# Optimization experiments

Hardware: AMD Instinct MI355X
Metric: run time of the kernel (lower is better)

## Reference

```python
import jax, jax.numpy as jnp
import numpy as np

B, T, E, H = 2, 2048, 1024, 16
Dh = E // H  # head_size = 64


def setup_inputs() -> dict:
    key = jax.random.key(0)
    ks = jax.random.split(key, 6)
    s = E ** -0.5
    x = jax.random.normal(ks[0], (B, T, E), dtype=jnp.float32)
    Wq = jax.random.normal(ks[1], (H, E, Dh), dtype=jnp.float32) * s
    Wk = jax.random.normal(ks[2], (H, E, Dh), dtype=jnp.float32) * s
    Wv = jax.random.normal(ks[3], (H, E, Dh), dtype=jnp.float32) * s
    wo_w = jax.random.normal(ks[4], (E, E), dtype=jnp.float32) * s  # torch Linear weight [out,in]
    wo_b = jax.random.normal(ks[5], (E,), dtype=jnp.float32) * 0.01
    return {"x": x, "Wq": Wq, "Wk": Wk, "Wv": Wv, "wo_w": wo_w, "wo_b": wo_b}


def reference(x, Wq, Wk, Wv, wo_w, wo_b):
    # Batched equivalent of the per-head Python loop: project all heads at once.
    q = jnp.einsum('bte,hed->bhtd', x, Wq)
    k = jnp.einsum('bte,hed->bhtd', x, Wk)
    v = jnp.einsum('bte,hed->bhtd', x, Wv)
    scale = Dh ** -0.5
    scores = jnp.einsum('bhtd,bhsd->bhts', q, k) * scale  # [B,H,T,T]
    causal = jnp.tril(jnp.ones((T, T), dtype=bool))
    scores = jnp.where(causal, scores, jnp.finfo(scores.dtype).min)
    att = jax.nn.softmax(scores, axis=-1)
    out = jnp.einsum('bhts,bhsd->bhtd', att, v)  # [B,H,T,Dh]
    # concat heads (head order along last dim, matching torch.cat over heads)
    out = out.transpose(0, 2, 1, 3).reshape(B, T, E)
    return out @ wo_w.T + wo_b
```

## Files before the change

### kernel.cpp

```cpp
#include <hip/hip_runtime.h>

#define B_ 2
#define T_ 2048
#define E_ 1024
#define H_ 16
#define DH 64

typedef unsigned short u16;
typedef unsigned int u32;
typedef __bf16 bf16x8 __attribute__((ext_vector_type(8)));
typedef float f32x4 __attribute__((ext_vector_type(4)));

__device__ __forceinline__ u16 f2bf(float f) {
  u32 u = __builtin_bit_cast(u32, f);
  u = u + 0x7FFFu + ((u >> 16) & 1u);
  return (u16)(u >> 16);
}
__device__ __forceinline__ bf16x8 ldfrag(const u16* p) { return *(const bf16x8*)p; }

__device__ __forceinline__ void gload_lds16(const u16* g, u16* l) {
  __builtin_amdgcn_global_load_lds((const __attribute__((address_space(1))) u32*)g,
                                   (__attribute__((address_space(3))) u32*)l, 16, 0, 0);
}

__global__ __launch_bounds__(256) void k_conv_all(const float* __restrict__ x,
                                                  const float* __restrict__ Wq,
                                                  const float* __restrict__ Wk,
                                                  const float* __restrict__ Wv,
                                                  const float* __restrict__ wo_w,
                                                  u16* __restrict__ xb, u16* __restrict__ wT,
                                                  u16* __restrict__ woB) {
  __shared__ __align__(16) u16 Ls[64][68];
  const int t = threadIdx.x;
  const int bx = blockIdx.x;
  if (bx < 2048 || bx >= 2816) {
    const float* src = (bx < 2048) ? x : wo_w;
    u16* dst = (bx < 2048) ? xb : woB;
    u32 i = (((bx < 2048) ? bx : (bx - 2816)) * 256u + t) * 8u;
    float4 a = *(const float4*)(src + i);
    float4 b = *(const float4*)(src + i + 4);
    uint4 v;
    v.x = (u32)f2bf(a.x) | ((u32)f2bf(a.y) << 16);
    v.y = (u32)f2bf(a.z) | ((u32)f2bf(a.w) << 16);
    v.z = (u32)f2bf(b.x) | ((u32)f2bf(b.y) << 16);
    v.w = (u32)f2bf(b.z) | ((u32)f2bf(b.w) << 16);
    *(uint4*)(dst + i) = v;
    return;
  }
  const int idx = bx - 2048;
  const int e0 = (idx & 15) * 64;
  const int h = (idx >> 4) & 15;
  const int which = idx >> 8;
  const float* src = (which == 0) ? Wq : ((which == 1) ? Wk : Wv);
  const float scale = (which == 0) ? 0.18033688011112042f : 1.0f;
#pragma unroll
  for (int p = 0; p < 4; p++) {
    int id2 = p * 256 + t;
    int row = id2 >> 4, ch = id2 & 15;
    float4 v = *(const float4*)(src + ((size_t)h * E_ + e0 + row) * DH + ch * 4);
    uint2 pk;
    pk.x = (u32)f2bf(v.x * scale) | ((u32)f2bf(v.y * scale) << 16);
    pk.y = (u32)f2bf(v.z * scale) | ((u32)f2bf(v.w * scale) << 16);
    *(uint2*)(&Ls[row][ch * 4]) = pk;
  }
  __syncthreads();
  u16* dst = wT + ((size_t)which * H_ + h) * (DH * E_);
#pragma unroll
  for (int p = 0; p < 4; p++) {
    int id2 = p * 256 + t;
    int d = id2 >> 4, ec = id2 & 15;
    uint2 pk;
    pk.x = (u32)Ls[ec * 4 + 0][d] | ((u32)Ls[ec * 4 + 1][d] << 16);
    pk.y = (u32)Ls[ec * 4 + 2][d] | ((u32)Ls[ec * 4 + 3][d] << 16);
    *(uint2*)(dst + (size_t)d * E_ + e0 + ec * 4) = pk;
  }
}

__global__ __launch_bounds__(256, 3) void k_qkv(const u16* __restrict__ xb, const u16* __restrict__ wT,
                                                u16* __restrict__ Qb, u16* __restrict__ Kb,
                                                u16* __restrict__ VbT) {
  __shared__ __align__(16) u16 As[128 * 64];
  __shared__ __align__(16) u16 Bs[128 * 64];
  const int tid = threadIdx.x;
  const int w = tid >> 6, lane = tid & 63, quad = lane >> 4, lr = lane & 15;
  const int wr = w >> 1, wc = w & 1;
  const int bid = blockIdx.x;
  const int xcd = bid & 7, bidx = bid >> 3;
  const int t0 = (xcd * 4 + bidx / 24) * 128;
  const int n0 = (bidx % 24) * 128;
  const int sr = lane >> 3, sc = lane & 7;

  f32x4 acc[4][4];
  const f32x4 z4 = {0.f, 0.f, 0.f, 0.f};
#pragma unroll
  for (int i = 0; i < 4; i++)
#pragma unroll
    for (int j = 0; j < 4; j++) acc[i][j] = z4;

  for (int k0 = 0; k0 < E_; k0 += 64) {
    __syncthreads();
#pragma unroll
    for (int ii = 0; ii < 4; ii++) {
      int ra = w * 32 + ii * 8 + sr;
      gload_lds16(xb + (size_t)(t0 + ra) * E_ + k0 + ((sc ^ (ra & 7)) << 3),
                  As + (w * 32 + ii * 8) * 64);
      gload_lds16(wT + (size_t)(n0 + ra) * E_ + k0 + ((sc ^ (ra & 7)) << 3),
                  Bs + (w * 32 + ii * 8) * 64);
    }
    __syncthreads();
#pragma unroll
    for (int kk = 0; kk < 2; kk++) {
      bf16x8 af[4], bfv[4];
#pragma unroll
      for (int rt = 0; rt < 4; rt++) {
        int row = wr * 64 + rt * 16 + lr;
        af[rt] = ldfrag(As + row * 64 + (((kk * 4 + quad) ^ (row & 7)) << 3));
      }
#pragma unroll
      for (int ct = 0; ct < 4; ct++) {
        int row = wc * 64 + ct * 16 + lr;
        bfv[ct] = ldfrag(Bs + row * 64 + (((kk * 4 + quad) ^ (row & 7)) << 3));
      }
#pragma unroll
      for (int rt = 0; rt < 4; rt++)
#pragma unroll
        for (int ct = 0; ct < 4; ct++)
          acc[rt][ct] = __builtin_amdgcn_mfma_f32_16x16x32_bf16(af[rt], bfv[ct], acc[rt][ct], 0, 0, 0);
    }
  }

  const int qkv = n0 >> 10;
  if (qkv < 2) {
    u16* outp = (qkv == 0) ? Qb : Kb;
#pragma unroll
    for (int rt = 0; rt < 4; rt++)
#pragma unroll
      for (int ct = 0; ct < 4; ct++) {
        int n = n0 + wc * 64 + ct * 16 + lr;
        int h = (n >> 6) & 15, d = n & 63;
#pragma unroll
        for (int r = 0; r < 4; r++) {
          int t = t0 + wr * 64 + rt * 16 + quad * 4 + r;
          int bb = t >> 11, tt = t & 2047;
          outp[(((size_t)bb * H_ + h) * T_ + tt) * DH + d] = f2bf(acc[rt][ct][r]);
        }
      }
  } else {
#pragma unroll
    for (int rt = 0; rt < 4; rt++)
#pragma unroll
      for (int ct = 0; ct < 4; ct++) {
        int n = n0 + wc * 64 + ct * 16 + lr;
        int h = (n >> 6) & 15, d = n & 63;
        int t = t0 + wr * 64 + rt * 16 + quad * 4;
        int bb = t >> 11, tt = t & 2047;
        uint2 pk;
        pk.x = (u32)f2bf(acc[rt][ct][0]) | ((u32)f2bf(acc[rt][ct][1]) << 16);
        pk.y = (u32)f2bf(acc[rt][ct][2]) | ((u32)f2bf(acc[rt][ct][3]) << 16);
        *(uint2*)(VbT + (((size_t)bb * H_ + h) * DH + d) * T_ + tt) = pk;
      }
  }
}

__global__ __launch_bounds__(256, 4) void k_attn(const u16* __restrict__ Qb, const u16* __restrict__ Kb,
                                                 const u16* __restrict__ VbT, u16* __restrict__ AO) {
  __shared__ __align__(16) u16 Ks[4096];
  __shared__ __align__(16) u16 Vts[4096];
  __shared__ __align__(16) u16 Ps[4096];
  const int tid = threadIdx.x;
  const int w = tid >> 6, lane = tid & 63, quad = lane >> 4, lr = lane & 15;
  const int l7 = lr & 7;
  const int srow = lane >> 3, schunk = lane & 7;
  const int i = blockIdx.x;
  const int h = blockIdx.y, bb = blockIdx.z;
  const u16* qb = Qb + ((size_t)bb * H_ + h) * (size_t)(T_ * DH);
  const u16* kb = Kb + ((size_t)bb * H_ + h) * (size_t)(T_ * DH);
  const u16* vbT = VbT + ((size_t)bb * H_ + h) * (size_t)(T_ * DH);
  const f32x4 z4 = {0.f, 0.f, 0.f, 0.f};
  const float MFIX = 20.0f;

  for (int jb = 0; jb < 2; jb++) {
    const int qt = jb ? i : (31 - i);
    const int t0 = qt * 64;

    const u16* qrow = qb + (size_t)(t0 + w * 16 + lr) * DH;
    bf16x8 bq0 = ldfrag(qrow + quad * 8);
    bf16x8 bq1 = ldfrag(qrow + 32 + quad * 8);

    f32x4 o_acc[4];
#pragma unroll
    for (int dt = 0; dt < 4; dt++) o_acc[dt] = z4;
    float l_i = 0.f;

    for (int jt = 0; jt <= qt; jt++) {
      const int j0 = jt * 64;
      __syncthreads();
#pragma unroll
      for (int ii = 0; ii < 2; ii++) {
        int r = w * 16 + ii * 8 + srow;
        gload_lds16(kb + (size_t)(j0 + r) * DH + ((schunk ^ (r & 7)) << 3),
                    Ks + (w * 16 + ii * 8) * 64);
        gload_lds16(vbT + (size_t)r * T_ + j0 + ((schunk ^ (r & 7)) << 3),
                    Vts + (w * 16 + ii * 8) * 64);
      }
      __syncthreads();

      f32x4 s_acc[4];
#pragma unroll
      for (int st = 0; st < 4; st++) s_acc[st] = z4;
#pragma unroll
      for (int st = 0; st < 4; st++) {
        bf16x8 ak0 = ldfrag(Ks + (st * 16 + lr) * 64 + ((quad ^ l7) << 3));
        bf16x8 ak1 = ldfrag(Ks + (st * 16 + lr) * 64 + (((4 + quad) ^ l7) << 3));
        s_acc[st] = __builtin_amdgcn_mfma_f32_16x16x32_bf16(ak0, bq0, s_acc[st], 0, 0, 0);
        s_acc[st] = __builtin_amdgcn_mfma_f32_16x16x32_bf16(ak1, bq1, s_acc[st], 0, 0, 0);
      }

      if (jt == qt) {
        int qloc = w * 16 + lr;
#pragma unroll
        for (int st = 0; st < 4; st++) {
          int sbase = st * 16 + quad * 4;
#pragma unroll
          for (int r = 0; r < 4; r++)
            if (sbase + r > qloc) s_acc[st][r] = -__builtin_inff();
        }
      }

      float rsum = 0.f;
#pragma unroll
      for (int st = 0; st < 4; st++) {
        float p0 = __builtin_amdgcn_exp2f(s_acc[st][0] - MFIX);
        float p1 = __builtin_amdgcn_exp2f(s_acc[st][1] - MFIX);
        float p2 = __builtin_amdgcn_exp2f(s_acc[st][2] - MFIX);
        float p3 = __builtin_amdgcn_exp2f(s_acc[st][3] - MFIX);
        rsum += (p0 + p1) + (p2 + p3);
        uint2 pk;
        pk.x = (__builtin_bit_cast(u32, p0) >> 16) | (__builtin_bit_cast(u32, p1) & 0xffff0000u);
        pk.y = (__builtin_bit_cast(u32, p2) >> 16) | (__builtin_bit_cast(u32, p3) & 0xffff0000u);
        *(uint2*)(Ps + (w * 16 + lr) * 64 + (((st * 2 + (quad >> 1)) ^ l7) << 3) + ((quad & 1) << 2)) = pk;
      }
      l_i += rsum;

#pragma unroll
      for (int kk = 0; kk < 2; kk++) {
        bf16x8 bp = ldfrag(Ps + (w * 16 + lr) * 64 + (((kk * 4 + quad) ^ l7) << 3));
#pragma unroll
        for (int dt = 0; dt < 4; dt++) {
          bf16x8 av = ldfrag(Vts + (dt * 16 + lr) * 64 + (((kk * 4 + quad) ^ l7) << 3));
          o_acc[dt] = __builtin_amdgcn_mfma_f32_16x16x32_bf16(av, bp, o_acc[dt], 0, 0, 0);
        }
      }
    }

    l_i += __shfl_xor(l_i, 16);
    l_i += __shfl_xor(l_i, 32);
    float inv = 1.0f / l_i;
    int t = t0 + w * 16 + lr;
    u16* orow = AO + ((size_t)bb * T_ + t) * E_ + h * DH;
#pragma unroll
    for (int dt = 0; dt < 4; dt++) {
      uint2 pk;
      pk.x = (u32)f2bf(o_acc[dt][0] * inv) | ((u32)f2bf(o_acc[dt][1] * inv) << 16);
      pk.y = (u32)f2bf(o_acc[dt][2] * inv) | ((u32)f2bf(o_acc[dt][3] * inv) << 16);
      *(uint2*)(orow + dt * 16 + quad * 4) = pk;
    }
  }
}

__global__ __launch_bounds__(256, 3) void k_oproj(const u16* __restrict__ AO, const u16* __restrict__ woB,
                                                  const float* __restrict__ bias, float* __restrict__ out) {
  __shared__ __align__(16) u16 As[128 * 64];
  __shared__ __align__(16) u16 Bs[64 * 64];
  const int tid = threadIdx.x;
  const int w = tid >> 6, lane = tid & 63, quad = lane >> 4, lr = lane & 15;
  const int wr = w >> 1, wc = w & 1;
  const int bid = blockIdx.x;
  const int xcd = bid & 7, bidx = bid >> 3;
  const int r0 = (xcd * 4 + (bidx >> 4)) * 128;
  const int n0 = (bidx & 15) * 64;
  const int sr = lane >> 3, sc = lane & 7;

  f32x4 acc[4][2];
  const f32x4 z4 = {0.f, 0.f, 0.f, 0.f};
#pragma unroll
  for (int i = 0; i < 4; i++) {
    acc[i][0] = z4;
    acc[i][1] = z4;
  }

  for (int k0 = 0; k0 < E_; k0 += 64) {
    __syncthreads();
#pragma unroll
    for (int ii = 0; ii < 4; ii++) {
      int ra = w * 32 + ii * 8 + sr;
      gload_lds16(AO + (size_t)(r0 + ra) * E_ + k0 + ((sc ^ (ra & 7)) << 3),
                  As + (w * 32 + ii * 8) * 64);
    }
#pragma unroll
    for (int ii = 0; ii < 2; ii++) {
      int rb = w * 16 + ii * 8 + sr;
      gload_lds16(woB + (size_t)(n0 + rb) * E_ + k0 + ((sc ^ (rb & 7)) << 3),
                  Bs + (w * 16 + ii * 8) * 64);
    }
    __syncthreads();
#pragma unroll
    for (int kk = 0; kk < 2; kk++) {
      bf16x8 af[4], bfv[2];
#pragma unroll
      for (int rt = 0; rt < 4; rt++) {
        int row = wr * 64 + rt * 16 + lr;
        af[rt] = ldfrag(As + row * 64 + (((kk * 4 + quad) ^ (row & 7)) << 3));
      }
#pragma unroll
      for (int ct = 0; ct < 2; ct++) {
        int row = wc * 32 + ct * 16 + lr;
        bfv[ct] = ldfrag(Bs + row * 64 + (((kk * 4 + quad) ^ (row & 7)) << 3));
      }
#pragma unroll
      for (int rt = 0; rt < 4; rt++)
#pragma unroll
        for (int ct = 0; ct < 2; ct++)
          acc[rt][ct] = __builtin_amdgcn_mfma_f32_16x16x32_bf16(af[rt], bfv[ct], acc[rt][ct], 0, 0, 0);
    }
  }

#pragma unroll
  for (int ct = 0; ct < 2; ct++) {
    int col = n0 + wc * 32 + ct * 16 + lr;
    float bv = bias[col];
#pragma unroll
    for (int rt = 0; rt < 4; rt++)
#pragma unroll
      for (int r = 0; r < 4; r++) {
        int row = r0 + wr * 64 + rt * 16 + quad * 4 + r;
        out[(size_t)row * E_ + col] = acc[rt][ct][r] + bv;
      }
  }
}

extern "C" void kernel_launch(void* const* d_in, const int* in_sizes, int n_in,
                              void* d_out, int out_size, void* d_ws, size_t ws_size,
                              hipStream_t stream) {
  const float* x = (const float*)d_in[0];
  const float* Wq = (const float*)d_in[1];
  const float* Wk = (const float*)d_in[2];
  const float* Wv = (const float*)d_in[3];
  const float* wo_w = (const float*)d_in[4];
  const float* wo_b = (const float*)d_in[5];
  float* out = (float*)d_out;
  char* ws = (char*)d_ws;

  u16* xb  = (u16*)(ws + 0);
  u16* wT  = (u16*)(ws + 8388608);
  u16* woB = (u16*)(ws + 14680064);
  u16* Qb  = (u16*)(ws + 16777216);
  u16* Kb  = (u16*)(ws + 25165824);
  u16* VbT = (u16*)(ws + 33554432);
  u16* AO  = (u16*)(ws + 41943040);

  k_conv_all<<<3328, 256, 0, stream>>>(x, Wq, Wk, Wv, wo_w, xb, wT, woB);
  k_qkv<<<768, 256, 0, stream>>>(xb, wT, Qb, Kb, VbT);
  k_attn<<<dim3(16, 16, 2), 256, 0, stream>>>(Qb, Kb, VbT, AO);
  k_oproj<<<512, 256, 0, stream>>>(AO, woB, wo_b, out);
}
```

Before: 179.9 us.

## Fuse all stages into one persistent kernel with software grid barriers

Replaces four separate kernel launches (conversion, QKV GEMM, attention, output projection) with one persistent 512-block kernel that runs each stage in turn, separated by atomic grid barriers. The barrier counters live in the output buffer, which is zeroed by a memset before launch. This removes launch gaps and inter-kernel drain, at the cost of imbalanced tile distribution (768 QKV tiles over 512 blocks), lower occupancy bounds, and barrier spin overhead. It relies on all 512 blocks being co-resident, and reuses the output memory for the barrier words.

Result: slower. 586.2 us (+225.9%).

```diff
diff --git a/kernel.cpp b/kernel.cpp
--- a/kernel.cpp
+++ b/kernel.cpp
@@ -23,319 +23,345 @@
                                    (__attribute__((address_space(3))) u32*)l, 16, 0, 0);
 }
 
-__global__ __launch_bounds__(256) void k_conv_all(const float* __restrict__ x,
-                                                  const float* __restrict__ Wq,
-                                                  const float* __restrict__ Wk,
-                                                  const float* __restrict__ Wv,
-                                                  const float* __restrict__ wo_w,
-                                                  u16* __restrict__ xb, u16* __restrict__ wT,
-                                                  u16* __restrict__ woB) {
-  __shared__ __align__(16) u16 Ls[64][68];
-  const int t = threadIdx.x;
-  const int bx = blockIdx.x;
-  if (bx < 2048 || bx >= 2816) {
-    const float* src = (bx < 2048) ? x : wo_w;
-    u16* dst = (bx < 2048) ? xb : woB;
-    u32 i = (((bx < 2048) ? bx : (bx - 2816)) * 256u + t) * 8u;
-    float4 a = *(const float4*)(src + i);
-    float4 b = *(const float4*)(src + i + 4);
-    uint4 v;
-    v.x = (u32)f2bf(a.x) | ((u32)f2bf(a.y) << 16);
-    v.y = (u32)f2bf(a.z) | ((u32)f2bf(a.w) << 16);
-    v.z = (u32)f2bf(b.x) | ((u32)f2bf(b.y) << 16);
-    v.w = (u32)f2bf(b.z) | ((u32)f2bf(b.w) << 16);
-    *(uint4*)(dst + i) = v;
-    return;
-  }
-  const int idx = bx - 2048;
-  const int e0 = (idx & 15) * 64;
-  const int h = (idx >> 4) & 15;
-  const int which = idx >> 8;
-  const float* src = (which == 0) ? Wq : ((which == 1) ? Wk : Wv);
-  const float scale = (which == 0) ? 0.18033688011112042f : 1.0f;
-#pragma unroll
-  for (int p = 0; p < 4; p++) {
-    int id2 = p * 256 + t;
-    int row = id2 >> 4, ch = id2 & 15;
-    float4 v = *(const float4*)(src + ((size_t)h * E_ + e0 + row) * DH + ch * 4);
-    uint2 pk;
-    pk.x = (u32)f2bf(v.x * scale) | ((u32)f2bf(v.y * scale) << 16);
-    pk.y = (u32)f2bf(v.z * scale) | ((u32)f2bf(v.w * scale) << 16);
-    *(uint2*)(&Ls[row][ch * 4]) = pk;
-  }
+__device__ __forceinline__ void grid_barrier(u32* bar, u32 nblk) {
   __syncthreads();
-  u16* dst = wT + ((size_t)which * H_ + h) * (DH * E_);
-#pragma unroll
-  for (int p = 0; p < 4; p++) {
-    int id2 = p * 256 + t;
-    int d = id2 >> 4, ec = id2 & 15;
-    uint2 pk;
-    pk.x = (u32)Ls[ec * 4 + 0][d] | ((u32)Ls[ec * 4 + 1][d] << 16);
-    pk.y = (u32)Ls[ec * 4 + 2][d] | ((u32)Ls[ec * 4 + 3][d] << 16);
-    *(uint2*)(dst + (size_t)d * E_ + e0 + ec * 4) = pk;
-  }
-}
-
-__global__ __launch_bounds__(256, 3) void k_qkv(const u16* __restrict__ xb, const u16* __restrict__ wT,
-                                                u16* __restrict__ Qb, u16* __restrict__ Kb,
-                                                u16* __restrict__ VbT) {
-  __shared__ __align__(16) u16 As[128 * 64];
-  __shared__ __align__(16) u16 Bs[128 * 64];
-  const int tid = threadIdx.x;
-  const int w = tid >> 6, lane = tid & 63, quad = lane >> 4, lr = lane & 15;
-  const int wr = w >> 1, wc = w & 1;
+  __threadfence();
+  if (threadIdx.x == 0) {
+    u32* cnt = bar;
+    u32* gen = bar + 32;
+    u32 g = __hip_atomic_load(gen, __ATOMIC_ACQUIRE, __HIP_MEMORY_SCOPE_AGENT);
+    u32 a = __hip_atomic_fetch_add(cnt, 1u, __ATOMIC_ACQ_REL, __HIP_MEMORY_SCOPE_AGENT);
+    if (a + 1u == nblk) {
+      __hip_atomic_store(cnt, 0u, __ATOMIC_RELAXED, __HIP_MEMORY_SCOPE_AGENT);
+      __hip_atomic_store(gen, g + 1u, __ATOMIC_RELEASE, __HIP_MEMORY_SCOPE_AGENT);
+    } else {
+      while (__hip_atomic_load(gen, __ATOMIC_ACQUIRE, __HIP_MEMORY_SCOPE_AGENT) == g)
+        __builtin_amdgcn_s_sleep(2);
+    }
+  }
+  __syncthreads();
+  __threadfence();
+}
+
+__global__ __launch_bounds__(256, 2) void k_mha(const float* __restrict__ x,
+                                                const float* __restrict__ Wq,
+                                                const float* __restrict__ Wk,
+                                                const float* __restrict__ Wv,
+                                                const float* __restrict__ wo_w,
+                                                const float* __restrict__ wo_b,
+                                                float* __restrict__ out,
+                                                char* __restrict__ ws) {
+  __shared__ __align__(16) u16 smem[16384];
+
+  u16* xb  = (u16*)(ws + 0);
+  u16* wT  = (u16*)(ws + 8388608);
+  u16* woB = (u16*)(ws + 14680064);
+  u16* Qb  = (u16*)(ws + 16777216);
+  u16* Kb  = (u16*)(ws + 25165824);
+  u16* VbT = (u16*)(ws + 33554432);
+  u16* AO  = (u16*)(ws + 41943040);
+  u32* bar = (u32*)out;
+
   const int bid = blockIdx.x;
-  const int xcd = bid & 7, bidx = bid >> 3;
-  const int t0 = (xcd * 4 + bidx / 24) * 128;
-  const int n0 = (bidx % 24) * 128;
-  const int sr = lane >> 3, sc = lane & 7;
-
-  f32x4 acc[4][4];
-  const f32x4 z4 = {0.f, 0.f, 0.f, 0.f};
-#pragma unroll
-  for (int i = 0; i < 4; i++)
-#pragma unroll
-    for (int j = 0; j < 4; j++) acc[i][j] = z4;
-
-  for (int k0 = 0; k0 < E_; k0 += 64) {
-    __syncthreads();
-#pragma unroll
-    for (int ii = 0; ii < 4; ii++) {
-      int ra = w * 32 + ii * 8 + sr;
-      gload_lds16(xb + (size_t)(t0 + ra) * E_ + k0 + ((sc ^ (ra & 7)) << 3),
-                  As + (w * 32 + ii * 8) * 64);
-      gload_lds16(wT + (size_t)(n0 + ra) * E_ + k0 + ((sc ^ (ra & 7)) << 3),
-                  Bs + (w * 32 + ii * 8) * 64);
-    }
-    __syncthreads();
-#pragma unroll
-    for (int kk = 0; kk < 2; kk++) {
-      bf16x8 af[4], bfv[4];
-#pragma unroll
-      for (int rt = 0; rt < 4; rt++) {
-        int row = wr * 64 + rt * 16 + lr;
-        af[rt] = ldfrag(As + row * 64 + (((kk * 4 + quad) ^ (row & 7)) << 3));
-      }
-#pragma unroll
-      for (int ct = 0; ct < 4; ct++) {
-        int row = wc * 64 + ct * 16 + lr;
-        bfv[ct] = ldfrag(Bs + row * 64 + (((kk * 4 + quad) ^ (row & 7)) << 3));
-      }
-#pragma unroll
-      for (int rt = 0; rt < 4; rt++)
-#pragma unroll
-        for (int ct = 0; ct < 4; ct++)
-          acc[rt][ct] = __builtin_amdgcn_mfma_f32_16x16x32_bf16(af[rt], bfv[ct], acc[rt][ct], 0, 0, 0);
-    }
-  }
-
-  const int qkv = n0 >> 10;
-  if (qkv < 2) {
-    u16* outp = (qkv == 0) ? Qb : Kb;
-#pragma unroll
-    for (int rt = 0; rt < 4; rt++)
-#pragma unroll
-      for (int ct = 0; ct < 4; ct++) {
-        int n = n0 + wc * 64 + ct * 16 + lr;
-        int h = (n >> 6) & 15, d = n & 63;
-#pragma unroll
-        for (int r = 0; r < 4; r++) {
-          int t = t0 + wr * 64 + rt * 16 + quad * 4 + r;
-          int bb = t >> 11, tt = t & 2047;
-          outp[(((size_t)bb * H_ + h) * T_ + tt) * DH + d] = f2bf(acc[rt][ct][r]);
-        }
-      }
-  } else {
-#pragma unroll
-    for (int rt = 0; rt < 4; rt++)
-#pragma unroll
-      for (int ct = 0; ct < 4; ct++) {
-        int n = n0 + wc * 64 + ct * 16 + lr;
-        int h = (n >> 6) & 15, d = n & 63;
-        int t = t0 + wr * 64 + rt * 16 + quad * 4;
-        int bb = t >> 11, tt = t & 2047;
-        uint2 pk;
-        pk.x = (u32)f2bf(acc[rt][ct][0]) | ((u32)f2bf(acc[rt][ct][1]) << 16);
-        pk.y = (u32)f2bf(acc[rt][ct][2]) | ((u32)f2bf(acc[rt][ct][3]) << 16);
-        *(uint2*)(VbT + (((size_t)bb * H_ + h) * DH + d) * T_ + tt) = pk;
-      }
-  }
-}
-
-__global__ __launch_bounds__(256, 4) void k_attn(const u16* __restrict__ Qb, const u16* __restrict__ Kb,
-                                                 const u16* __restrict__ VbT, u16* __restrict__ AO) {
-  __shared__ __align__(16) u16 Ks[4096];
-  __shared__ __align__(16) u16 Vts[4096];
-  __shared__ __align__(16) u16 Ps[4096];
   const int tid = threadIdx.x;
   const int w = tid >> 6, lane = tid & 63, quad = lane >> 4, lr = lane & 15;
   const int l7 = lr & 7;
-  const int srow = lane >> 3, schunk = lane & 7;
-  const int i = blockIdx.x;
-  const int h = blockIdx.y, bb = blockIdx.z;
-  const u16* qb = Qb + ((size_t)bb * H_ + h) * (size_t)(T_ * DH);
-  const u16* kb = Kb + ((size_t)bb * H_ + h) * (size_t)(T_ * DH);
-  const u16* vbT = VbT + ((size_t)bb * H_ + h) * (size_t)(T_ * DH);
+  const int sr = lane >> 3, sc = lane & 7;
   const f32x4 z4 = {0.f, 0.f, 0.f, 0.f};
-  const float MFIX = 20.0f;
-
-  for (int jb = 0; jb < 2; jb++) {
-    const int qt = jb ? i : (31 - i);
-    const int t0 = qt * 64;
-
-    const u16* qrow = qb + (size_t)(t0 + w * 16 + lr) * DH;
-    bf16x8 bq0 = ldfrag(qrow + quad * 8);
-    bf16x8 bq1 = ldfrag(qrow + 32 + quad * 8);
-
-    f32x4 o_acc[4];
-#pragma unroll
-    for (int dt = 0; dt < 4; dt++) o_acc[dt] = z4;
-    float l_i = 0.f;
-
-    for (int jt = 0; jt <= qt; jt++) {
-      const int j0 = jt * 64;
-      __syncthreads();
+
+  for (int u = bid; u < 3328; u += 512) {
+    if (u < 2048 || u >= 2816) {
+      const float* src = (u < 2048) ? x : wo_w;
+      u16* dst = (u < 2048) ? xb : woB;
+      u32 i = (((u < 2048) ? u : (u - 2816)) * 256u + tid) * 8u;
+      float4 a = *(const float4*)(src + i);
+      float4 b = *(const float4*)(src + i + 4);
+      uint4 v;
+      v.x = (u32)f2bf(a.x) | ((u32)f2bf(a.y) << 16);
+      v.y = (u32)f2bf(a.z) | ((u32)f2bf(a.w) << 16);
+      v.z = (u32)f2bf(b.x) | ((u32)f2bf(b.y) << 16);
+      v.w = (u32)f2bf(b.z) | ((u32)f2bf(b.w) << 16);
+      *(uint4*)(dst + i) = v;
+    } else {
+      const int idx = u - 2048;
+      const int e0 = (idx & 15) * 64;
+      const int h = (idx >> 4) & 15;
+      const int which = idx >> 8;
+      const float* src = (which == 0) ? Wq : ((which == 1) ? Wk : Wv);
+      const float scale = (which == 0) ? 0.18033688011112042f : 1.0f;
+      __syncthreads();
+#pragma unroll
+      for (int p = 0; p < 4; p++) {
+        int id2 = p * 256 + tid;
+        int row = id2 >> 4, ch = id2 & 15;
+        float4 v = *(const float4*)(src + ((size_t)h * E_ + e0 + row) * DH + ch * 4);
+        uint2 pk;
+        pk.x = (u32)f2bf(v.x * scale) | ((u32)f2bf(v.y * scale) << 16);
+        pk.y = (u32)f2bf(v.z * scale) | ((u32)f2bf(v.w * scale) << 16);
+        *(uint2*)(smem + row * 68 + ch * 4) = pk;
+      }
+      __syncthreads();
+      u16* dst = wT + ((size_t)which * H_ + h) * (DH * E_);
+#pragma unroll
+      for (int p = 0; p < 4; p++) {
+        int id2 = p * 256 + tid;
+        int d = id2 >> 4, ec = id2 & 15;
+        uint2 pk;
+        pk.x = (u32)smem[(ec * 4 + 0) * 68 + d] | ((u32)smem[(ec * 4 + 1) * 68 + d] << 16);
+        pk.y = (u32)smem[(ec * 4 + 2) * 68 + d] | ((u32)smem[(ec * 4 + 3) * 68 + d] << 16);
+        *(uint2*)(dst + (size_t)d * E_ + e0 + ec * 4) = pk;
+      }
+    }
+  }
+
+  grid_barrier(bar, 512);
+
+  for (int tile = bid; tile < 768; tile += 512) {
+    u16* As = smem;
+    u16* Bs = smem + 8192;
+    const int wr = w >> 1, wc = w & 1;
+    const int xcd = tile & 7, bidx = tile >> 3;
+    const int t0 = (xcd * 4 + bidx / 24) * 128;
+    const int n0 = (bidx % 24) * 128;
+
+    f32x4 acc[4][4];
+#pragma unroll
+    for (int i = 0; i < 4; i++)
+#pragma unroll
+      for (int j = 0; j < 4; j++) acc[i][j] = z4;
+
+    for (int k0 = 0; k0 < E_; k0 += 64) {
+      __syncthreads();
+#pragma unroll
+      for (int ii = 0; ii < 4; ii++) {
+        int ra = w * 32 + ii * 8 + sr;
+        gload_lds16(xb + (size_t)(t0 + ra) * E_ + k0 + ((sc ^ (ra & 7)) << 3),
+                    As + (w * 32 + ii * 8) * 64);
+        gload_lds16(wT + (size_t)(n0 + ra) * E_ + k0 + ((sc ^ (ra & 7)) << 3),
+                    Bs + (w * 32 + ii * 8) * 64);
+      }
+      __syncthreads();
+#pragma unroll
+      for (int kk = 0; kk < 2; kk++) {
+        bf16x8 af[4], bfv[4];
+#pragma unroll
+        for (int rt = 0; rt < 4; rt++) {
+          int row = wr * 64 + rt * 16 + lr;
+          af[rt] = ldfrag(As + row * 64 + (((kk * 4 + quad) ^ (row & 7)) << 3));
+        }
+#pragma unroll
+        for (int ct = 0; ct < 4; ct++) {
+          int row = wc * 64 + ct * 16 + lr;
+          bfv[ct] = ldfrag(Bs + row * 64 + (((kk * 4 + quad) ^ (row & 7)) << 3));
+        }
+#pragma unroll
+        for (int rt = 0; rt < 4; rt++)
+#pragma unroll
+          for (int ct = 0; ct < 4; ct++)
+            acc[rt][ct] = __builtin_amdgcn_mfma_f32_16x16x32_bf16(af[rt], bfv[ct], acc[rt][ct], 0, 0, 0);
+      }
+    }
+
+    const int qkv = n0 >> 10;
+    if (qkv < 2) {
+      u16* outp = (qkv == 0) ? Qb : Kb;
+#pragma unroll
+      for (int rt = 0; rt < 4; rt++)
+#pragma unroll
+        for (int ct = 0; ct < 4; ct++) {
+          int n = n0 + wc * 64 + ct * 16 + lr;
+          int h = (n >> 6) & 15, d = n & 63;
+#pragma unroll
+          for (int r = 0; r < 4; r++) {
+            int t = t0 + wr * 64 + rt * 16 + quad * 4 + r;
+            int bb = t >> 11, tt = t & 2047;
+            outp[(((size_t)bb * H_ + h) * T_ + tt) * DH + d] = f2bf(acc[rt][ct][r]);
+          }
+        }
+    } else {
+#pragma unroll
+      for (int rt = 0; rt < 4; rt++)
+#pragma unroll
+        for (int ct = 0; ct < 4; ct++) {
+          int n = n0 + wc * 64 + ct * 16 + lr;
+          int h = (n >> 6) & 15, d = n & 63;
+          int t = t0 + wr * 64 + rt * 16 + quad * 4;
+          int bb = t >> 11, tt = t & 2047;
+          uint2 pk;
+          pk.x = (u32)f2bf(acc[rt][ct][0]) | ((u32)f2bf(acc[rt][ct][1]) << 16);
+          pk.y = (u32)f2bf(acc[rt][ct][2]) | ((u32)f2bf(acc[rt][ct][3]) << 16);
+          *(uint2*)(VbT + (((size_t)bb * H_ + h) * DH + d) * T_ + tt) = pk;
+        }
+    }
+  }
+
+  grid_barrier(bar, 512);
+
+  {
+    u16* Ks  = smem;
+    u16* Vts = smem + 4096;
+    u16* Ps  = smem + 8192;
+    const int i = bid & 15;
+    const int h = (bid >> 4) & 15, bb = bid >> 8;
+    const u16* qb = Qb + ((size_t)bb * H_ + h) * (size_t)(T_ * DH);
+    const u16* kb = Kb + ((size_t)bb * H_ + h) * (size_t)(T_ * DH);
+    const u16* vbT = VbT + ((size_t)bb * H_ + h) * (size_t)(T_ * DH);
+    const float MFIX = 20.0f;
+
+    for (int jb = 0; jb < 2; jb++) {
+      const int qt = jb ? i : (31 - i);
+      const int t0 = qt * 64;
+
+      const u16* qrow = qb + (size_t)(t0 + w * 16 + lr) * DH;
+      bf16x8 bq0 = ldfrag(qrow + quad * 8);
+      bf16x8 bq1 = ldfrag(qrow + 32 + quad * 8);
+
+      f32x4 o_acc[4];
+#pragma unroll
+      for (int dt = 0; dt < 4; dt++) o_acc[dt] = z4;
+      float l_i = 0.f;
+
+      for (int jt = 0; jt <= qt; jt++) {
+        const int j0 = jt * 64;
+        __syncthreads();
+#pragma unroll
+        for (int ii = 0; ii < 2; ii++) {
+          int r = w * 16 + ii * 8 + sr;
+          gload_lds16(kb + (size_t)(j0 + r) * DH + ((sc ^ (r & 7)) << 3),
+                      Ks + (w * 16 + ii * 8) * 64);
+          gload_lds16(vbT + (size_t)r * T_ + j0 + ((sc ^ (r & 7)) << 3),
+                      Vts + (w * 16 + ii * 8) * 64);
+        }
+        __syncthreads();
+
+        f32x4 s_acc[4];
+#pragma unroll
+        for (int st = 0; st < 4; st++) s_acc[st] = z4;
+#pragma unroll
+        for (int st = 0; st < 4; st++) {
+          bf16x8 ak0 = ldfrag(Ks + (st * 16 + lr) * 64 + ((quad ^ l7) << 3));
+          bf16x8 ak1 = ldfrag(Ks + (st * 16 + lr) * 64 + (((4 + quad) ^ l7) << 3));
+          s_acc[st] = __builtin_amdgcn_mfma_f32_16x16x32_bf16(ak0, bq0, s_acc[st], 0, 0, 0);
+          s_acc[st] = __builtin_amdgcn_mfma_f32_16x16x32_bf16(ak1, bq1, s_acc[st], 0, 0, 0);
+        }
+
+        if (jt == qt) {
+          int qloc = w * 16 + lr;
+#pragma unroll
+          for (int st = 0; st < 4; st++) {
+            int sbase = st * 16 + quad * 4;
+#pragma unroll
+            for (int r = 0; r < 4; r++)
+              if (sbase + r > qloc) s_acc[st][r] = -__builtin_inff();
+          }
+        }
+
+        float rsum = 0.f;
+#pragma unroll
+        for (int st = 0; st < 4; st++) {
+          float p0 = __builtin_amdgcn_exp2f(s_acc[st][0] - MFIX);
+          float p1 = __builtin_amdgcn_exp2f(s_acc[st][1] - MFIX);
+          float p2 = __builtin_amdgcn_exp2f(s_acc[st][2] - MFIX);
+          float p3 = __builtin_amdgcn_exp2f(s_acc[st][3] - MFIX);
+          rsum += (p0 + p1) + (p2 + p3);
+          uint2 pk;
+          pk.x = (__builtin_bit_cast(u32, p0) >> 16) | (__builtin_bit_cast(u32, p1) & 0xffff0000u);
+          pk.y = (__builtin_bit_cast(u32, p2) >> 16) | (__builtin_bit_cast(u32, p3) & 0xffff0000u);
+          *(uint2*)(Ps + (w * 16 + lr) * 64 + (((st * 2 + (quad >> 1)) ^ l7) << 3) + ((quad & 1) << 2)) = pk;
+        }
+        l_i += rsum;
+
+#pragma unroll
+        for (int kk = 0; kk < 2; kk++) {
+          bf16x8 bp = ldfrag(Ps + (w * 16 + lr) * 64 + (((kk * 4 + quad) ^ l7) << 3));
+#pragma unroll
+          for (int dt = 0; dt < 4; dt++) {
+            bf16x8 av = ldfrag(Vts + (dt * 16 + lr) * 64 + (((kk * 4 + quad) ^ l7) << 3));
+            o_acc[dt] = __builtin_amdgcn_mfma_f32_16x16x32_bf16(av, bp, o_acc[dt], 0, 0, 0);
+          }
+        }
+      }
+
+      l_i += __shfl_xor(l_i, 16);
+      l_i += __shfl_xor(l_i, 32);
+      float inv = 1.0f / l_i;
+      int t = t0 + w * 16 + lr;
+      u16* orow = AO + ((size_t)bb * T_ + t) * E_ + h * DH;
+#pragma unroll
+      for (int dt = 0; dt < 4; dt++) {
+        uint2 pk;
+        pk.x = (u32)f2bf(o_acc[dt][0] * inv) | ((u32)f2bf(o_acc[dt][1] * inv) << 16);
+        pk.y = (u32)f2bf(o_acc[dt][2] * inv) | ((u32)f2bf(o_acc[dt][3] * inv) << 16);
+        *(uint2*)(orow + dt * 16 + quad * 4) = pk;
+      }
+    }
+  }
+
+  grid_barrier(bar, 512);
+
+  {
+    u16* As = smem;
+    u16* Bs = smem + 8192;
+    const int wr = w >> 1, wc = w & 1;
+    const int xcd = bid & 7, bidx = bid >> 3;
+    const int r0 = (xcd * 4 + (bidx >> 4)) * 128;
+    const int n0 = (bidx & 15) * 64;
+
+    f32x4 acc[4][2];
+#pragma unroll
+    for (int i = 0; i < 4; i++) {
+      acc[i][0] = z4;
+      acc[i][1] = z4;
+    }
+
+    for (int k0 = 0; k0 < E_; k0 += 64) {
+      __syncthreads();
+#pragma unroll
+      for (int ii = 0; ii < 4; ii++) {
+        int ra = w * 32 + ii * 8 + sr;
+        gload_lds16(AO + (size_t)(r0 + ra) * E_ + k0 + ((sc ^ (ra & 7)) << 3),
+                    As + (w * 32 + ii * 8) * 64);
+      }
 #pragma unroll
       for (int ii = 0; ii < 2; ii++) {
-        int r = w * 16 + ii * 8 + srow;
-        gload_lds16(kb + (size_t)(j0 + r) * DH + ((schunk ^ (r & 7)) << 3),
-                    Ks + (w * 16 + ii * 8) * 64);
-        gload_lds16(vbT + (size_t)r * T_ + j0 + ((schunk ^ (r & 7)) << 3),
-                    Vts + (w * 16 + ii * 8) * 64);
-      }
-      __syncthreads();
-
-      f32x4 s_acc[4];
-#pragma unroll
-      for (int st = 0; st < 4; st++) s_acc[st] = z4;
-#pragma unroll
-      for (int st = 0; st < 4; st++) {
-        bf16x8 ak0 = ldfrag(Ks + (st * 16 + lr) * 64 + ((quad ^ l7) << 3));
-        bf16x8 ak1 = ldfrag(Ks + (st * 16 + lr) * 64 + (((4 + quad) ^ l7) << 3));
-        s_acc[st] = __builtin_amdgcn_mfma_f32_16x16x32_bf16(ak0, bq0, s_acc[st], 0, 0, 0);
-        s_acc[st] = __builtin_amdgcn_mfma_f32_16x16x32_bf16(ak1, bq1, s_acc[st], 0, 0, 0);
-      }
-
-      if (jt == qt) {
-        int qloc = w * 16 + lr;
-#pragma unroll
-        for (int st = 0; st < 4; st++) {
-          int sbase = st * 16 + quad * 4;
-#pragma unroll
-          for (int r = 0; r < 4; r++)
-            if (sbase + r > qloc) s_acc[st][r] = -__builtin_inff();
-        }
-      }
-
-      float rsum = 0.f;
-#pragma unroll
-      for (int st = 0; st < 4; st++) {
-        float p0 = __builtin_amdgcn_exp2f(s_acc[st][0] - MFIX);
-        float p1 = __builtin_amdgcn_exp2f(s_acc[st][1] - MFIX);
-        float p2 = __builtin_amdgcn_exp2f(s_acc[st][2] - MFIX);
-        float p3 = __builtin_amdgcn_exp2f(s_acc[st][3] - MFIX);
-        rsum += (p0 + p1) + (p2 + p3);
-        uint2 pk;
-        pk.x = (__builtin_bit_cast(u32, p0) >> 16) | (__builtin_bit_cast(u32, p1) & 0xffff0000u);
-        pk.y = (__builtin_bit_cast(u32, p2) >> 16) | (__builtin_bit_cast(u32, p3) & 0xffff0000u);
-        *(uint2*)(Ps + (w * 16 + lr) * 64 + (((st * 2 + (quad >> 1)) ^ l7) << 3) + ((quad & 1) << 2)) = pk;
-      }
-      l_i += rsum;
-
+        int rb = w * 16 + ii * 8 + sr;
+        gload_lds16(woB + (size_t)(n0 + rb) * E_ + k0 + ((sc ^ (rb & 7)) << 3),
+                    Bs + (w * 16 + ii * 8) * 64);
+      }
+      __syncthreads();
 #pragma unroll
       for (int kk = 0; kk < 2; kk++) {
-        bf16x8 bp = ldfrag(Ps + (w * 16 + lr) * 64 + (((kk * 4 + quad) ^ l7) << 3));
-#pragma unroll
-        for (int dt = 0; dt < 4; dt++) {
-          bf16x8 av = ldfrag(Vts + (dt * 16 + lr) * 64 + (((kk * 4 + quad) ^ l7) << 3));
-          o_acc[dt] = __builtin_amdgcn_mfma_f32_16x16x32_bf16(av, bp, o_acc[dt], 0, 0, 0);
-        }
-      }
-    }
-
-    l_i += __shfl_xor(l_i, 16);
-    l_i += __shfl_xor(l_i, 32);
-    float inv = 1.0f / l_i;
-    int t = t0 + w * 16 + lr;
-    u16* orow = AO + ((size_t)bb * T_ + t) * E_ + h * DH;
-#pragma unroll
-    for (int dt = 0; dt < 4; dt++) {
-      uint2 pk;
-      pk.x = (u32)f2bf(o_acc[dt][0] * inv) | ((u32)f2bf(o_acc[dt][1] * inv) << 16);
-      pk.y = (u32)f2bf(o_acc[dt][2] * inv) | ((u32)f2bf(o_acc[dt][3] * inv) << 16);
-      *(uint2*)(orow + dt * 16 + quad * 4) = pk;
-    }
-  }
-}
-
-__global__ __launch_bounds__(256, 3) void k_oproj(const u16* __restrict__ AO, const u16* __restrict__ woB,
-                                                  const float* __restrict__ bias, float* __restrict__ out) {
-  __shared__ __align__(16) u16 As[128 * 64];
-  __shared__ __align__(16) u16 Bs[64 * 64];
-  const int tid = threadIdx.x;
-  const int w = tid >> 6, lane = tid & 63, quad = lane >> 4, lr = lane & 15;
-  const int wr = w >> 1, wc = w & 1;
-  const int bid = blockIdx.x;
-  const int xcd = bid & 7, bidx = bid >> 3;
-  const int r0 = (xcd * 4 + (bidx >> 4)) * 128;
-  const int n0 = (bidx & 15) * 64;
-  const int sr = lane >> 3, sc = lane & 7;
-
-  f32x4 acc[4][2];
-  const f32x4 z4 = {0.f, 0.f, 0.f, 0.f};
-#pragma unroll
-  for (int i = 0; i < 4; i++) {
-    acc[i][0] = z4;
-    acc[i][1] = z4;
-  }
-
-  for (int k0 = 0; k0 < E_; k0 += 64) {
-    __syncthreads();
-#pragma unroll
-    for (int ii = 0; ii < 4; ii++) {
-      int ra = w * 32 + ii * 8 + sr;
-      gload_lds16(AO + (size_t)(r0 + ra) * E_ + k0 + ((sc ^ (ra & 7)) << 3),
-                  As + (w * 32 + ii * 8) * 64);
-    }
-#pragma unroll
-    for (int ii = 0; ii < 2; ii++) {
-      int rb = w * 16 + ii * 8 + sr;
-      gload_lds16(woB + (size_t)(n0 + rb) * E_ + k0 + ((sc ^ (rb & 7)) << 3),
-                  Bs + (w * 16 + ii * 8) * 64);
-    }
-    __syncthreads();
-#pragma unroll
-    for (int kk = 0; kk < 2; kk++) {
-      bf16x8 af[4], bfv[2];
-#pragma unroll
-      for (int rt = 0; rt < 4; rt++) {
-        int row = wr * 64 + rt * 16 + lr;
-        af[rt] = ldfrag(As + row * 64 + (((kk * 4 + quad) ^ (row & 7)) << 3));
-      }
-#pragma unroll
-      for (int ct = 0; ct < 2; ct++) {
-        int row = wc * 32 + ct * 16 + lr;
-        bfv[ct] = ldfrag(Bs + row * 64 + (((kk * 4 + quad) ^ (row & 7)) << 3));
-      }
+        bf16x8 af[4], bfv[2];
+#pragma unroll
+        for (int rt = 0; rt < 4; rt++) {
+          int row = wr * 64 + rt * 16 + lr;
+          af[rt] = ldfrag(As + row * 64 + (((kk * 4 + quad) ^ (row & 7)) << 3));
+        }
+#pragma unroll
+        for (int ct = 0; ct < 2; ct++) {
+          int row = wc * 32 + ct * 16 + lr;
+          bfv[ct] = ldfrag(Bs + row * 64 + (((kk * 4 + quad) ^ (row & 7)) << 3));
+        }
+#pragma unroll
+        for (int rt = 0; rt < 4; rt++)
+#pragma unroll
+          for (int ct = 0; ct < 2; ct++)
+            acc[rt][ct] = __builtin_amdgcn_mfma_f32_16x16x32_bf16(af[rt], bfv[ct], acc[rt][ct], 0, 0, 0);
+      }
+    }
+
+#pragma unroll
+    for (int ct = 0; ct < 2; ct++) {
+      int col = n0 + wc * 32 + ct * 16 + lr;
+      float bv = wo_b[col];
 #pragma unroll
       for (int rt = 0; rt < 4; rt++)
 #pragma unroll
-        for (int ct = 0; ct < 2; ct++)
-          acc[rt][ct] = __builtin_amdgcn_mfma_f32_16x16x32_bf16(af[rt], bfv[ct], acc[rt][ct], 0, 0, 0);
-    }
-  }
-
-#pragma unroll
-  for (int ct = 0; ct < 2; ct++) {
-    int col = n0 + wc * 32 + ct * 16 + lr;
-    float bv = bias[col];
-#pragma unroll
-    for (int rt = 0; rt < 4; rt++)
-#pragma unroll
-      for (int r = 0; r < 4; r++) {
-        int row = r0 + wr * 64 + rt * 16 + quad * 4 + r;
-        out[(size_t)row * E_ + col] = acc[rt][ct][r] + bv;
-      }
+        for (int r = 0; r < 4; r++) {
+          int row = r0 + wr * 64 + rt * 16 + quad * 4 + r;
+          out[(size_t)row * E_ + col] = acc[rt][ct][r] + bv;
+        }
+    }
   }
 }
 
@@ -351,16 +377,6 @@
   float* out = (float*)d_out;
   char* ws = (char*)d_ws;
 
-  u16* xb  = (u16*)(ws + 0);
-  u16* wT  = (u16*)(ws + 8388608);
-  u16* woB = (u16*)(ws + 14680064);
-  u16* Qb  = (u16*)(ws + 16777216);
-  u16* Kb  = (u16*)(ws + 25165824);
-  u16* VbT = (u16*)(ws + 33554432);
-  u16* AO  = (u16*)(ws + 41943040);
-
-  k_conv_all<<<3328, 256, 0, stream>>>(x, Wq, Wk, Wv, wo_w, xb, wT, woB);
-  k_qkv<<<768, 256, 0, stream>>>(xb, wT, Qb, Kb, VbT);
-  k_attn<<<dim3(16, 16, 2), 256, 0, stream>>>(Qb, Kb, VbT, AO);
-  k_oproj<<<512, 256, 0, stream>>>(AO, woB, wo_b, out);
-}
+  hipMemsetAsync(d_out, 0, 256, stream);
+  k_mha<<<512, 256, 0, stream>>>(x, Wq, Wk, Wv, wo_w, wo_b, out, ws);
+}
```

## Double-buffer K/V tiles in attention kernel and raise MFMA wave priority

Applied to the files above, without the earlier changes.

The attention kernel now keeps two LDS buffers for K and V^T. The next tile's async global-to-LDS loads are issued before computing on the current tile, and the per-iteration barriers drop from two to one. The QK^T and PV MFMA sections are wrapped in s_setprio to favour matrix work. Launch bounds drop from 4 to 2 blocks per CU to accommodate the larger LDS footprint and register use. The goal is to hide K/V load latency behind compute, at the cost of extra LDS and possibly lower occupancy.

Result: faster. 170.7 us (-5.1%).

```diff
diff --git a/kernel.cpp b/kernel.cpp
--- a/kernel.cpp
+++ b/kernel.cpp
@@ -162,10 +162,10 @@
   }
 }
 
-__global__ __launch_bounds__(256, 4) void k_attn(const u16* __restrict__ Qb, const u16* __restrict__ Kb,
+__global__ __launch_bounds__(256, 2) void k_attn(const u16* __restrict__ Qb, const u16* __restrict__ Kb,
                                                  const u16* __restrict__ VbT, u16* __restrict__ AO) {
-  __shared__ __align__(16) u16 Ks[4096];
-  __shared__ __align__(16) u16 Vts[4096];
+  __shared__ __align__(16) u16 Ks[2][4096];
+  __shared__ __align__(16) u16 Vts[2][4096];
   __shared__ __align__(16) u16 Ps[4096];
   const int tid = threadIdx.x;
   const int w = tid >> 6, lane = tid & 63, quad = lane >> 4, lr = lane & 15;
@@ -192,29 +192,42 @@
     for (int dt = 0; dt < 4; dt++) o_acc[dt] = z4;
     float l_i = 0.f;
 
+#pragma unroll
+    for (int ii = 0; ii < 2; ii++) {
+      int r = w * 16 + ii * 8 + srow;
+      gload_lds16(kb + (size_t)r * DH + ((schunk ^ (r & 7)) << 3),
+                  &Ks[0][(w * 16 + ii * 8) * 64]);
+      gload_lds16(vbT + (size_t)r * T_ + ((schunk ^ (r & 7)) << 3),
+                  &Vts[0][(w * 16 + ii * 8) * 64]);
+    }
+    __syncthreads();
+
+    int cur = 0;
     for (int jt = 0; jt <= qt; jt++) {
-      const int j0 = jt * 64;
-      __syncthreads();
-#pragma unroll
-      for (int ii = 0; ii < 2; ii++) {
-        int r = w * 16 + ii * 8 + srow;
-        gload_lds16(kb + (size_t)(j0 + r) * DH + ((schunk ^ (r & 7)) << 3),
-                    Ks + (w * 16 + ii * 8) * 64);
-        gload_lds16(vbT + (size_t)r * T_ + j0 + ((schunk ^ (r & 7)) << 3),
-                    Vts + (w * 16 + ii * 8) * 64);
-      }
-      __syncthreads();
+      if (jt < qt) {
+        const int jn = (jt + 1) * 64;
+#pragma unroll
+        for (int ii = 0; ii < 2; ii++) {
+          int r = w * 16 + ii * 8 + srow;
+          gload_lds16(kb + (size_t)(jn + r) * DH + ((schunk ^ (r & 7)) << 3),
+                      &Ks[cur ^ 1][(w * 16 + ii * 8) * 64]);
+          gload_lds16(vbT + (size_t)r * T_ + jn + ((schunk ^ (r & 7)) << 3),
+                      &Vts[cur ^ 1][(w * 16 + ii * 8) * 64]);
+        }
+      }
 
       f32x4 s_acc[4];
 #pragma unroll
       for (int st = 0; st < 4; st++) s_acc[st] = z4;
+      __builtin_amdgcn_s_setprio(1);
 #pragma unroll
       for (int st = 0; st < 4; st++) {
-        bf16x8 ak0 = ldfrag(Ks + (st * 16 + lr) * 64 + ((quad ^ l7) << 3));
-        bf16x8 ak1 = ldfrag(Ks + (st * 16 + lr) * 64 + (((4 + quad) ^ l7) << 3));
+        bf16x8 ak0 = ldfrag(&Ks[cur][(st * 16 + lr) * 64 + ((quad ^ l7) << 3)]);
+        bf16x8 ak1 = ldfrag(&Ks[cur][(st * 16 + lr) * 64 + (((4 + quad) ^ l7) << 3)]);
         s_acc[st] = __builtin_amdgcn_mfma_f32_16x16x32_bf16(ak0, bq0, s_acc[st], 0, 0, 0);
         s_acc[st] = __builtin_amdgcn_mfma_f32_16x16x32_bf16(ak1, bq1, s_acc[st], 0, 0, 0);
       }
+      __builtin_amdgcn_s_setprio(0);
 
       if (jt == qt) {
         int qloc = w * 16 + lr;
@@ -242,15 +255,20 @@
       }
       l_i += rsum;
 
+      __builtin_amdgcn_s_setprio(1);
 #pragma unroll
       for (int kk = 0; kk < 2; kk++) {
         bf16x8 bp = ldfrag(Ps + (w * 16 + lr) * 64 + (((kk * 4 + quad) ^ l7) << 3));
 #pragma unroll
         for (int dt = 0; dt < 4; dt++) {
-          bf16x8 av = ldfrag(Vts + (dt * 16 + lr) * 64 + (((kk * 4 + quad) ^ l7) << 3));
+          bf16x8 av = ldfrag(&Vts[cur][(dt * 16 + lr) * 64 + (((kk * 4 + quad) ^ l7) << 3)]);
           o_acc[dt] = __builtin_amdgcn_mfma_f32_16x16x32_bf16(av, bp, o_acc[dt], 0, 0, 0);
         }
       }
+      __builtin_amdgcn_s_setprio(0);
+
+      __syncthreads();
+      cur ^= 1;
     }
 
     l_i += __shfl_xor(l_i, 16);
```

## Switch attention to 32x32x16 MFMA with key-split waves and register P exchange

Applied to the files above, without the earlier changes.

The attention kernel now uses 32x32x16 bf16 MFMA tiles. The four waves split into two query halves and two key halves, and the P matrix is passed between lane halves with shuffles instead of a shared-memory round trip. Partial outputs and row sums from the two key-half waves are combined through shared memory at the end of each query tile, and s_setprio is raised around the MFMA sections. The aim is fewer LDS operations and instructions per MFMA. In exchange the kernel uses more registers and has lower occupancy (launch bounds drop from 4 to 2 blocks) plus an extra reduction step with barriers.

After: 175.9 us. 1.02x faster.

```diff
diff --git a/kernel.cpp b/kernel.cpp
--- a/kernel.cpp
+++ b/kernel.cpp
@@ -10,6 +10,7 @@
 typedef unsigned int u32;
 typedef __bf16 bf16x8 __attribute__((ext_vector_type(8)));
 typedef float f32x4 __attribute__((ext_vector_type(4)));
+typedef float f32x16 __attribute__((ext_vector_type(16)));
 
 __device__ __forceinline__ u16 f2bf(float f) {
   u32 u = __builtin_bit_cast(u32, f);
@@ -162,34 +163,37 @@
   }
 }
 
-__global__ __launch_bounds__(256, 4) void k_attn(const u16* __restrict__ Qb, const u16* __restrict__ Kb,
+__global__ __launch_bounds__(256, 2) void k_attn(const u16* __restrict__ Qb, const u16* __restrict__ Kb,
                                                  const u16* __restrict__ VbT, u16* __restrict__ AO) {
-  __shared__ __align__(16) u16 Ks[4096];
-  __shared__ __align__(16) u16 Vts[4096];
-  __shared__ __align__(16) u16 Ps[4096];
+  __shared__ __align__(16) u16 smem[8192];
+  __shared__ float Ll[128];
+  u16* Ks = smem;
+  u16* Vts = smem + 4096;
+  float* Lo = (float*)smem;
+
   const int tid = threadIdx.x;
-  const int w = tid >> 6, lane = tid & 63, quad = lane >> 4, lr = lane & 15;
-  const int l7 = lr & 7;
+  const int w = tid >> 6, lane = tid & 63;
+  const int l31 = lane & 31, hi = lane >> 5;
+  const int qhalf = w & 1, shalf = w >> 1;
   const int srow = lane >> 3, schunk = lane & 7;
   const int i = blockIdx.x;
   const int h = blockIdx.y, bb = blockIdx.z;
   const u16* qb = Qb + ((size_t)bb * H_ + h) * (size_t)(T_ * DH);
   const u16* kb = Kb + ((size_t)bb * H_ + h) * (size_t)(T_ * DH);
   const u16* vbT = VbT + ((size_t)bb * H_ + h) * (size_t)(T_ * DH);
-  const f32x4 z4 = {0.f, 0.f, 0.f, 0.f};
   const float MFIX = 20.0f;
 
   for (int jb = 0; jb < 2; jb++) {
     const int qt = jb ? i : (31 - i);
     const int t0 = qt * 64;
-
-    const u16* qrow = qb + (size_t)(t0 + w * 16 + lr) * DH;
-    bf16x8 bq0 = ldfrag(qrow + quad * 8);
-    bf16x8 bq1 = ldfrag(qrow + 32 + quad * 8);
-
-    f32x4 o_acc[4];
-#pragma unroll
-    for (int dt = 0; dt < 4; dt++) o_acc[dt] = z4;
+    const int q_abs = t0 + qhalf * 32 + l31;
+
+    const u16* qrow = qb + (size_t)q_abs * DH;
+    bf16x8 bq[4];
+#pragma unroll
+    for (int ki = 0; ki < 4; ki++) bq[ki] = ldfrag(qrow + ki * 16 + hi * 8);
+
+    f32x16 o0 = {}, o1 = {};
     float l_i = 0.f;
 
     for (int jt = 0; jt <= qt; jt++) {
@@ -205,65 +209,109 @@
       }
       __syncthreads();
 
-      f32x4 s_acc[4];
-#pragma unroll
-      for (int st = 0; st < 4; st++) s_acc[st] = z4;
-#pragma unroll
-      for (int st = 0; st < 4; st++) {
-        bf16x8 ak0 = ldfrag(Ks + (st * 16 + lr) * 64 + ((quad ^ l7) << 3));
-        bf16x8 ak1 = ldfrag(Ks + (st * 16 + lr) * 64 + (((4 + quad) ^ l7) << 3));
-        s_acc[st] = __builtin_amdgcn_mfma_f32_16x16x32_bf16(ak0, bq0, s_acc[st], 0, 0, 0);
-        s_acc[st] = __builtin_amdgcn_mfma_f32_16x16x32_bf16(ak1, bq1, s_acc[st], 0, 0, 0);
-      }
+      f32x16 s_acc = {};
+      const int krow = shalf * 32 + l31;
+      __builtin_amdgcn_s_setprio(1);
+#pragma unroll
+      for (int ki = 0; ki < 4; ki++) {
+        bf16x8 ak = ldfrag(Ks + krow * 64 + (((2 * ki + hi) ^ (krow & 7)) << 3));
+        s_acc = __builtin_amdgcn_mfma_f32_32x32x16_bf16(ak, bq[ki], s_acc, 0, 0, 0);
+      }
+      __builtin_amdgcn_s_setprio(0);
 
       if (jt == qt) {
-        int qloc = w * 16 + lr;
-#pragma unroll
-        for (int st = 0; st < 4; st++) {
-          int sbase = st * 16 + quad * 4;
-#pragma unroll
-          for (int r = 0; r < 4; r++)
-            if (sbase + r > qloc) s_acc[st][r] = -__builtin_inff();
+#pragma unroll
+        for (int r16 = 0; r16 < 16; r16++) {
+          int s_abs = j0 + shalf * 32 + (r16 & 3) + 8 * (r16 >> 2) + 4 * hi;
+          if (s_abs > q_abs) s_acc[r16] = -__builtin_inff();
         }
       }
 
+      float p[16];
       float rsum = 0.f;
 #pragma unroll
-      for (int st = 0; st < 4; st++) {
-        float p0 = __builtin_amdgcn_exp2f(s_acc[st][0] - MFIX);
-        float p1 = __builtin_amdgcn_exp2f(s_acc[st][1] - MFIX);
-        float p2 = __builtin_amdgcn_exp2f(s_acc[st][2] - MFIX);
-        float p3 = __builtin_amdgcn_exp2f(s_acc[st][3] - MFIX);
-        rsum += (p0 + p1) + (p2 + p3);
+      for (int r16 = 0; r16 < 16; r16++) {
+        p[r16] = __builtin_amdgcn_exp2f(s_acc[r16] - MFIX);
+        rsum += p[r16];
+      }
+      l_i += rsum;
+
+      u32 a[8], xch[8];
+#pragma unroll
+      for (int g = 0; g < 8; g++)
+        a[g] = (__builtin_bit_cast(u32, p[2 * g]) >> 16) |
+               (__builtin_bit_cast(u32, p[2 * g + 1]) & 0xffff0000u);
+#pragma unroll
+      for (int g = 0; g < 8; g++) xch[g] = __shfl_xor(a[g], 32);
+
+      __builtin_amdgcn_s_setprio(1);
+#pragma unroll
+      for (int ks = 0; ks < 2; ks++) {
+        uint4 fu;
+        fu.x = hi ? xch[4 * ks + 2] : a[4 * ks + 0];
+        fu.y = hi ? xch[4 * ks + 3] : a[4 * ks + 1];
+        fu.z = hi ? a[4 * ks + 2] : xch[4 * ks + 0];
+        fu.w = hi ? a[4 * ks + 3] : xch[4 * ks + 1];
+        bf16x8 bp = __builtin_bit_cast(bf16x8, fu);
+        const int ch = shalf * 4 + ks * 2 + hi;
+        {
+          int vrow = l31;
+          bf16x8 av = ldfrag(Vts + vrow * 64 + ((ch ^ (vrow & 7)) << 3));
+          o0 = __builtin_amdgcn_mfma_f32_32x32x16_bf16(av, bp, o0, 0, 0, 0);
+        }
+        {
+          int vrow = 32 + l31;
+          bf16x8 av = ldfrag(Vts + vrow * 64 + ((ch ^ (vrow & 7)) << 3));
+          o1 = __builtin_amdgcn_mfma_f32_32x32x16_bf16(av, bp, o1, 0, 0, 0);
+        }
+      }
+      __builtin_amdgcn_s_setprio(0);
+    }
+
+    __syncthreads();
+    if (shalf) {
+      float* base = Lo + qhalf * 2048 + lane * 32;
+#pragma unroll
+      for (int g = 0; g < 4; g++) {
+        float4 v = {o0[4 * g + 0], o0[4 * g + 1], o0[4 * g + 2], o0[4 * g + 3]};
+        *(float4*)(base + ((g ^ (lane & 7)) << 2)) = v;
+      }
+#pragma unroll
+      for (int g = 4; g < 8; g++) {
+        float4 v = {o1[4 * g - 16], o1[4 * g - 15], o1[4 * g - 14], o1[4 * g - 13]};
+        *(float4*)(base + ((g ^ (lane & 7)) << 2)) = v;
+      }
+      Ll[qhalf * 64 + lane] = l_i;
+    }
+    __syncthreads();
+    if (!shalf) {
+      float* base = Lo + qhalf * 2048 + lane * 32;
+#pragma unroll
+      for (int g = 0; g < 4; g++) {
+        float4 v = *(float4*)(base + ((g ^ (lane & 7)) << 2));
+        o0[4 * g + 0] += v.x; o0[4 * g + 1] += v.y;
+        o0[4 * g + 2] += v.z; o0[4 * g + 3] += v.w;
+      }
+#pragma unroll
+      for (int g = 4; g < 8; g++) {
+        float4 v = *(float4*)(base + ((g ^ (lane & 7)) << 2));
+        o1[4 * g - 16] += v.x; o1[4 * g - 15] += v.y;
+        o1[4 * g - 14] += v.z; o1[4 * g - 13] += v.w;
+      }
+      l_i += Ll[qhalf * 64 + lane];
+      l_i += __shfl_xor(l_i, 32);
+      float inv = 1.0f / l_i;
+      u16* orow = AO + ((size_t)bb * T_ + q_abs) * E_ + h * DH;
+#pragma unroll
+      for (int g = 0; g < 4; g++) {
         uint2 pk;
-        pk.x = (__builtin_bit_cast(u32, p0) >> 16) | (__builtin_bit_cast(u32, p1) & 0xffff0000u);
-        pk.y = (__builtin_bit_cast(u32, p2) >> 16) | (__builtin_bit_cast(u32, p3) & 0xffff0000u);
-        *(uint2*)(Ps + (w * 16 + lr) * 64 + (((st * 2 + (quad >> 1)) ^ l7) << 3) + ((quad & 1) << 2)) = pk;
-      }
-      l_i += rsum;
-
-#pragma unroll
-      for (int kk = 0; kk < 2; kk++) {
-        bf16x8 bp = ldfrag(Ps + (w * 16 + lr) * 64 + (((kk * 4 + quad) ^ l7) << 3));
-#pragma unroll
-        for (int dt = 0; dt < 4; dt++) {
-          bf16x8 av = ldfrag(Vts + (dt * 16 + lr) * 64 + (((kk * 4 + quad) ^ l7) << 3));
-          o_acc[dt] = __builtin_amdgcn_mfma_f32_16x16x32_bf16(av, bp, o_acc[dt], 0, 0, 0);
-        }
-      }
-    }
-
-    l_i += __shfl_xor(l_i, 16);
-    l_i += __shfl_xor(l_i, 32);
-    float inv = 1.0f / l_i;
-    int t = t0 + w * 16 + lr;
-    u16* orow = AO + ((size_t)bb * T_ + t) * E_ + h * DH;
-#pragma unroll
-    for (int dt = 0; dt < 4; dt++) {
-      uint2 pk;
-      pk.x = (u32)f2bf(o_acc[dt][0] * inv) | ((u32)f2bf(o_acc[dt][1] * inv) << 16);
-      pk.y = (u32)f2bf(o_acc[dt][2] * inv) | ((u32)f2bf(o_acc[dt][3] * inv) << 16);
-      *(uint2*)(orow + dt * 16 + quad * 4) = pk;
+        pk.x = (u32)f2bf(o0[4 * g + 0] * inv) | ((u32)f2bf(o0[4 * g + 1] * inv) << 16);
+        pk.y = (u32)f2bf(o0[4 * g + 2] * inv) | ((u32)f2bf(o0[4 * g + 3] * inv) << 16);
+        *(uint2*)(orow + 8 * g + 4 * hi) = pk;
+        pk.x = (u32)f2bf(o1[4 * g + 0] * inv) | ((u32)f2bf(o1[4 * g + 1] * inv) << 16);
+        pk.y = (u32)f2bf(o1[4 * g + 2] * inv) | ((u32)f2bf(o1[4 * g + 3] * inv) << 16);
+        *(uint2*)(orow + 32 + 8 * g + 4 * hi) = pk;
+      }
     }
   }
 }
```
